# Kernel tuning notes

Measured on AMD Instinct MI355X. Metric: run time of the kernel, lower is better.

Reference implementation:

```python
import jax, jax.numpy as jnp
import numpy as np

L, D, H, DH, W, G, FF = 2, 768, 12, 64, 256, 64, 3072  # W = one-sided window (attention_window=512)
B, S = 2, 4096
NEG = -1e9


def setup_inputs() -> dict:
    key = jax.random.key(0)
    ks = jax.random.split(key, 16)
    inp = {}
    inp['hidden_states'] = jax.random.normal(ks[0], (B, S, D), jnp.float32)
    # HF Longformer convention: <0 masked, >0 global, 0 local. First G tokens are global.
    inp['attention_mask'] = jnp.zeros((B, S), jnp.float32).at[:, :G].set(1.0)
    inp['padding_len'] = 0
    inp['level_hierarchy'] = 0
    def w(k, shape):
        return (jax.random.normal(k, shape, jnp.float32) * 0.02)
    for i, n in enumerate(['Wq', 'Wk', 'Wv', 'Wqg', 'Wkg', 'Wvg', 'Wo']):
        inp[n] = w(ks[1 + i], (L, D, D))
        inp['b' + n[1:].lower()] = jnp.zeros((L, D), jnp.float32)
    inp['Wi'] = w(ks[8], (L, D, FF)); inp['bi'] = jnp.zeros((L, FF), jnp.float32)
    inp['Wo2'] = w(ks[9], (L, FF, D)); inp['bo2'] = jnp.zeros((L, D), jnp.float32)
    for n in ['ln1', 'ln2']:
        inp[n + '_g'] = jnp.ones((L, D), jnp.float32)
        inp[n + '_b'] = jnp.zeros((L, D), jnp.float32)
    return inp


def _ln(x, g, b):
    mu = jnp.mean(x, -1, keepdims=True)
    var = jnp.mean(jnp.square(x - mu), -1, keepdims=True)
    return (x - mu) * jax.lax.rsqrt(var + 1e-5) * g + b


def _chunk3(x, nc, w):
    # x: [..., S, d] -> [..., nc, 3w, d]: keys of chunks (c-1, c, c+1), zero-padded at the ends
    shp = x.shape
    xr = x.reshape(shp[:-2] + (nc, w, shp[-1]))
    pad = [(0, 0)] * xr.ndim
    pad[-3] = (1, 1)
    xp = jnp.pad(xr, pad)
    return jnp.concatenate([xp[..., :-2, :, :], xp[..., 1:-1, :, :], xp[..., 2:, :, :]], axis=-2)


def _layer(h, mask, Wq, bq, Wk, bk, Wv, bv, Wqg, bqg, Wkg, bkg, Wvg, bvg,
           Wo, bo, ln1_g, ln1_b, Wi, bi, Wo2, bo2, ln2_g, ln2_b):
    Bb, Ss, Dd = h.shape
    nc = Ss // W
    scale = 1.0 / np.sqrt(DH)
    def heads(x):
        return x.reshape(Bb, Ss, H, DH).transpose(0, 2, 1, 3)  # [B,H,S,dh]
    q = heads(h @ Wq + bq) * scale
    k = heads(h @ Wk + bk)
    v = heads(h @ Wv + bv)
    # --- sliding-window (banded) attention, chunked ---
    qc = q.reshape(Bb, H, nc, W, DH)
    k3 = _chunk3(k, nc, W)  # [B,H,nc,3W,dh]
    v3 = _chunk3(v, nc, W)
    local = jnp.einsum('bhcid,bhcjd->bhcij', qc, k3)  # [B,H,nc,W,3W]
    i = jnp.arange(W)[:, None]
    j = jnp.arange(3 * W)[None, :]
    band_ok = jnp.abs(j - W - i) <= W                              # [W,3W]
    keypos = jnp.arange(nc)[:, None, None] * W + (j - W)[None]     # [nc,1,3W]
    in_range = (keypos >= 0) & (keypos < Ss)
    # masked and global keys are removed from the windowed attention (handled via global cols)
    key_local = _chunk3((mask == 0).astype(h.dtype)[..., None], nc, W)[..., 0] > 0.5  # [B,nc,3W]
    valid = band_ok[None, None] & in_range[None] & key_local[:, :, None, :]  # [B,nc,W,3W]
    local = jnp.where(valid[:, None], local, NEG)
    # --- global key columns (every token attends to the G global tokens) ---
    kg, vg = k[:, :, :G], v[:, :, :G]
    sg = jnp.einsum('bhsd,bhgd->bhsg', q, kg).reshape(Bb, H, nc, W, G)
    probs = jax.nn.softmax(jnp.concatenate([sg, local], axis=-1), axis=-1)
    pg, pl = probs[..., :G], probs[..., G:]
    out = (jnp.einsum('bhcig,bhgd->bhcid', pg, vg)
           + jnp.einsum('bhcij,bhcjd->bhcid', pl, v3)).reshape(Bb, H, Ss, DH)
    # --- global token rows: full attention with dedicated global projections ---
    qg = heads(h @ Wqg + bqg)[:, :, :G] * scale
    kgf = heads(h @ Wkg + bkg)
    vgf = heads(h @ Wvg + bvg)
    add = jnp.where(mask < 0, NEG, 0.0)[:, None, None, :]
    pgl = jax.nn.softmax(jnp.einsum('bhgd,bhsd->bhgs', qg, kgf) + add, axis=-1)
    out = out.at[:, :, :G].set(jnp.einsum('bhgs,bhsd->bhgd', pgl, vgf))
    out = jnp.where((mask < 0)[:, None, :, None], 0.0, out)
    attn = out.transpose(0, 2, 1, 3).reshape(Bb, Ss, Dd) @ Wo + bo
    h = _ln(attn + h, ln1_g, ln1_b)
    ff = jax.nn.gelu(h @ Wi + bi, approximate=False) @ Wo2 + bo2
    return _ln(ff + h, ln2_g, ln2_b)


def reference(hidden_states, attention_mask, padding_len, level_hierarchy,
              Wq, bq, Wk, bk, Wv, bv, Wqg, bqg, Wkg, bkg, Wvg, bvg,
              Wo, bo, ln1_g, ln1_b, Wi, bi, Wo2, bo2, ln2_g, ln2_b):
    h = hidden_states
    for l in range(L):
        h = _layer(h, attention_mask,
                   Wq[l], bq[l], Wk[l], bk[l], Wv[l], bv[l],
                   Wqg[l], bqg[l], Wkg[l], bkg[l], Wvg[l], bvg[l],
                   Wo[l], bo[l], ln1_g[l], ln1_b[l],
                   Wi[l], bi[l], Wo2[l], bo2[l], ln2_g[l], ln2_b[l])
    if padding_len > 0:
        h = h[:, :-padding_len]
    return h
```

## Files before the change

kernel.cpp:

```cpp
#include <hip/hip_runtime.h>

#define B_ 2
#define S_ 4096
#define D_ 768
#define H_ 12
#define DH_ 64
#define W_ 256
#define G_ 64
#define FF_ 3072
#define L_ 2
#define M_ (B_*S_)
#define NEGV -1e9f
#define NSPLIT 16

typedef short bf16x8 __attribute__((ext_vector_type(8)));
typedef float f32x4 __attribute__((ext_vector_type(4)));
typedef unsigned short u16;
typedef unsigned short u16x4 __attribute__((ext_vector_type(4)));

__device__ __forceinline__ u16 f2bf(float f) {
  union { float f; unsigned u; } a; a.f = f;
  unsigned r = a.u + 0x7FFFu + ((a.u >> 16) & 1u);
  return (u16)(r >> 16);
}
__device__ __forceinline__ float b2f(u16 u) {
  union { unsigned u; float f; } a; a.u = ((unsigned)u) << 16;
  return a.f;
}

__device__ __forceinline__ f32x4 mfma16(bf16x8 a, bf16x8 b, f32x4 c) {
  return __builtin_amdgcn_mfma_f32_16x16x32_bf16(a, b, c, 0, 0, 0);
}

__device__ __forceinline__ void gload16(const u16* g, u16* l) {
  __builtin_amdgcn_global_load_lds((const __attribute__((address_space(1))) void*)g,
                                   (__attribute__((address_space(3))) void*)l, 16, 0, 0);
}

__device__ __forceinline__ int xcd_swz(int bid, int nwg) {
  if ((nwg & 7) == 0) {
    int cpx = nwg >> 3;
    bid = (bid & 7) * cpx + (bid >> 3);
  }
  return bid;
}

struct Ptr7 { const float* p[7]; };
__global__ __launch_bounds__(256) void wtrans7(Ptr7 in, u16* __restrict__ out) {
  __shared__ float tile[32][33];
  int z = blockIdx.z;
  int slab = z >> 1, l = z & 1;
  const float* src = in.p[slab] + (size_t)l * D_ * D_;
  u16* dst = out + (size_t)z * D_ * D_;
  int k0 = blockIdx.y * 32, n0 = blockIdx.x * 32;
  int tx = threadIdx.x, ty = threadIdx.y;
#pragma unroll
  for (int i = 0; i < 4; i++)
    tile[ty + i*8][tx] = src[(size_t)(k0 + ty + i*8) * D_ + n0 + tx];
  __syncthreads();
#pragma unroll
  for (int i = 0; i < 4; i++)
    dst[(size_t)(n0 + ty + i*8) * D_ + k0 + tx] = f2bf(tile[tx][ty + i*8]);
}

__global__ __launch_bounds__(256) void wtrans(const float* __restrict__ in,
                                              u16* __restrict__ out, int K, int N) {
  __shared__ float tile[32][33];
  size_t base = (size_t)blockIdx.z * K * N;
  int k0 = blockIdx.y * 32, n0 = blockIdx.x * 32;
  int tx = threadIdx.x, ty = threadIdx.y;
#pragma unroll
  for (int i = 0; i < 4; i++)
    tile[ty + i*8][tx] = in[base + (size_t)(k0 + ty + i*8) * N + n0 + tx];
  __syncthreads();
#pragma unroll
  for (int i = 0; i < 4; i++)
    out[base + (size_t)(n0 + ty + i*8) * K + k0 + tx] = f2bf(tile[tx][ty + i*8]);
}

__global__ __launch_bounds__(256) void conv_b(const float* __restrict__ in,
                                              u16* __restrict__ outb, int n4) {
  int i = blockIdx.x * 256 + threadIdx.x;
  if (i >= n4) return;
  float4 v = ((const float4*)in)[i];
  u16x4 o;
  o[0] = f2bf(v.x); o[1] = f2bf(v.y); o[2] = f2bf(v.z); o[3] = f2bf(v.w);
  ((u16x4*)outb)[i] = o;
}

template <int MODE>
__device__ __forceinline__ float epi_post(float v) {
  if (MODE == 2) return v * 0.125f;
  if (MODE == 3) {
    float y = 0.79788456f * (v + 0.044715f * v * v * v);
    float e = __expf(fminf(2.f * y, 20.f));
    return v * e / (e + 1.f);
  }
  return v;
}

template <int MODE>
__global__ __launch_bounds__(256) void gemm_pipe(const u16* __restrict__ A,
                                                 const u16* __restrict__ Bt,
                                                 const float* __restrict__ bias,
                                                 u16* __restrict__ Cb,
                                                 int Ndim, int Kdim, int rowTileStride) {
  __shared__ u16 sA[2][4096];
  __shared__ u16 sB[2][4096];
  int gx = gridDim.x;
  int bid = blockIdx.x + blockIdx.y * gx;
  bid = xcd_swz(bid, gx * gridDim.y);
  int bm = (bid / gx) * rowTileStride * 128;
  int bn = (bid % gx) * 128;
  int tid = threadIdx.x;
  int lane = tid & 63, w = tid >> 6;
  int r0w = (w >> 1) * 64, c0w = (w & 1) * 64;
  int lr = lane & 15, lg = lane >> 4;

  int f0 = tid, l0 = f0 >> 3, s0 = (f0 & 7) ^ (l0 & 7);
  int row0 = (l0 << 1) | (s0 >> 2), c0s = (s0 & 3) * 8;
  int f1 = tid + 256, l1 = f1 >> 3, s1 = (f1 & 7) ^ (l1 & 7);
  int row1 = (l1 << 1) | (s1 >> 2), c1s = (s1 & 3) * 8;
  const u16* A0 = A + (size_t)(bm + row0) * Kdim + c0s;
  const u16* A1 = A + (size_t)(bm + row1) * Kdim + c1s;
  const u16* B0 = Bt + (size_t)(bn + row0) * Kdim + c0s;
  const u16* B1 = Bt + (size_t)(bn + row1) * Kdim + c1s;

  int offa[4], offb[4];
#pragma unroll
  for (int i = 0; i < 4; i++) {
    int ra = r0w + i * 16 + lr;
    int la = ra >> 1, sa = ((ra & 1) << 2) | lg;
    offa[i] = la * 64 + (sa ^ (la & 7)) * 8;
    int rb = c0w + i * 16 + lr;
    int lb = rb >> 1, sb = ((rb & 1) << 2) | lg;
    offb[i] = lb * 64 + (sb ^ (lb & 7)) * 8;
  }

  int nt = Kdim >> 5;
  f32x4 acc[4][4] = {};

  gload16(A0, &sA[0][tid * 8]);
  gload16(A1, &sA[0][tid * 8 + 2048]);
  gload16(B0, &sB[0][tid * 8]);
  gload16(B1, &sB[0][tid * 8 + 2048]);

  for (int t = 0; t < nt; t++) {
    int cur = t & 1;
    if (t + 1 < nt) {
      int k1 = (t + 1) << 5;
      gload16(A0 + k1, &sA[cur ^ 1][tid * 8]);
      gload16(A1 + k1, &sA[cur ^ 1][tid * 8 + 2048]);
      gload16(B0 + k1, &sB[cur ^ 1][tid * 8]);
      gload16(B1 + k1, &sB[cur ^ 1][tid * 8 + 2048]);
      asm volatile("s_waitcnt vmcnt(4)" ::: "memory");
    } else {
      asm volatile("s_waitcnt vmcnt(0)" ::: "memory");
    }
    __builtin_amdgcn_s_barrier();
    __builtin_amdgcn_sched_barrier(0);
    bf16x8 a[4], b[4];
#pragma unroll
    for (int i = 0; i < 4; i++) a[i] = *(const bf16x8*)&sA[cur][offa[i]];
#pragma unroll
    for (int j = 0; j < 4; j++) b[j] = *(const bf16x8*)&sB[cur][offb[j]];
#pragma unroll
    for (int i = 0; i < 4; i++)
#pragma unroll
      for (int j = 0; j < 4; j++)
        acc[i][j] = mfma16(a[i], b[j], acc[i][j]);
    __builtin_amdgcn_sched_barrier(0);
    __builtin_amdgcn_s_barrier();
    __builtin_amdgcn_sched_barrier(0);
  }

  int r0 = bm + r0w, c0 = bn + c0w;
  int cr = (lane >> 4) * 4, cc = lane & 15;
#pragma unroll
  for (int j = 0; j < 4; j++) {
    int col = c0 + j * 16 + cc;
    float bv = bias[col];
#pragma unroll
    for (int i = 0; i < 4; i++)
#pragma unroll
      for (int r = 0; r < 4; r++) {
        size_t off = (size_t)(r0 + i * 16 + cr + r) * Ndim + col;
        Cb[off] = f2bf(epi_post<MODE>(acc[i][j][r] + bv));
      }
  }
}

struct Bias5 { const float* p[5]; };
__global__ __launch_bounds__(256) void gemm_qkv(const u16* __restrict__ A,
                                                const u16* __restrict__ Wt,
                                                Bias5 bp,
                                                u16* __restrict__ OutBase,
                                                int l) {
  __shared__ u16 sA[2][4096];
  __shared__ u16 sB[2][4096];
  int bid = blockIdx.x + blockIdx.y * 30;
  bid = xcd_swz(bid, 1920);
  int bx = bid % 30, by = bid / 30;
  int widx = bx / 6;
  int bn = (bx % 6) * 128;
  int bm = by * 128;
  int slab = widx + (widx >= 3 ? 1 : 0);
  const size_t DD = (size_t)D_ * D_;
  const u16* Bt = Wt + ((size_t)slab * L_ + l) * DD;
  u16* Cb = OutBase + (size_t)slab * M_ * D_;
  const float* bias = bp.p[widx];
  int tid = threadIdx.x;
  int lane = tid & 63, w = tid >> 6;
  int r0w = (w >> 1) * 64, c0w = (w & 1) * 64;
  int lr = lane & 15, lg = lane >> 4;

  int f0 = tid, l0 = f0 >> 3, s0 = (f0 & 7) ^ (l0 & 7);
  int row0 = (l0 << 1) | (s0 >> 2), c0s = (s0 & 3) * 8;
  int f1 = tid + 256, l1 = f1 >> 3, s1 = (f1 & 7) ^ (l1 & 7);
  int row1 = (l1 << 1) | (s1 >> 2), c1s = (s1 & 3) * 8;
  const u16* A0 = A + (size_t)(bm + row0) * D_ + c0s;
  const u16* A1 = A + (size_t)(bm + row1) * D_ + c1s;
  const u16* B0 = Bt + (size_t)(bn + row0) * D_ + c0s;
  const u16* B1 = Bt + (size_t)(bn + row1) * D_ + c1s;

  int offa[4], offb[4];
#pragma unroll
  for (int i = 0; i < 4; i++) {
    int ra = r0w + i * 16 + lr;
    int la = ra >> 1, sa = ((ra & 1) << 2) | lg;
    offa[i] = la * 64 + (sa ^ (la & 7)) * 8;
    int rb = c0w + i * 16 + lr;
    int lb = rb >> 1, sb = ((rb & 1) << 2) | lg;
    offb[i] = lb * 64 + (sb ^ (lb & 7)) * 8;
  }

  const int nt = D_ >> 5;
  f32x4 acc[4][4] = {};

  gload16(A0, &sA[0][tid * 8]);
  gload16(A1, &sA[0][tid * 8 + 2048]);
  gload16(B0, &sB[0][tid * 8]);
  gload16(B1, &sB[0][tid * 8 + 2048]);

  for (int t = 0; t < nt; t++) {
    int cur = t & 1;
    if (t + 1 < nt) {
      int k1 = (t + 1) << 5;
      gload16(A0 + k1, &sA[cur ^ 1][tid * 8]);
      gload16(A1 + k1, &sA[cur ^ 1][tid * 8 + 2048]);
      gload16(B0 + k1, &sB[cur ^ 1][tid * 8]);
      gload16(B1 + k1, &sB[cur ^ 1][tid * 8 + 2048]);
      asm volatile("s_waitcnt vmcnt(4)" ::: "memory");
    } else {
      asm volatile("s_waitcnt vmcnt(0)" ::: "memory");
    }
    __builtin_amdgcn_s_barrier();
    __builtin_amdgcn_sched_barrier(0);
    bf16x8 a[4], b[4];
#pragma unroll
    for (int i = 0; i < 4; i++) a[i] = *(const bf16x8*)&sA[cur][offa[i]];
#pragma unroll
    for (int j = 0; j < 4; j++) b[j] = *(const bf16x8*)&sB[cur][offb[j]];
#pragma unroll
    for (int i = 0; i < 4; i++)
#pragma unroll
      for (int j = 0; j < 4; j++)
        acc[i][j] = mfma16(a[i], b[j], acc[i][j]);
    __builtin_amdgcn_sched_barrier(0);
    __builtin_amdgcn_s_barrier();
    __builtin_amdgcn_sched_barrier(0);
  }

  int r0 = bm + r0w, c0 = bn + c0w;
  int cr = (lane >> 4) * 4, cc = lane & 15;
  float scale = (widx == 0) ? 0.125f : 1.0f;
#pragma unroll
  for (int j = 0; j < 4; j++) {
    int col = c0 + j * 16 + cc;
    float bv = bias[col];
#pragma unroll
    for (int i = 0; i < 4; i++)
#pragma unroll
      for (int r = 0; r < 4; r++) {
        size_t off = (size_t)(r0 + i * 16 + cr + r) * D_ + col;
        Cb[off] = f2bf((acc[i][j][r] + bv) * scale);
      }
  }
}

__global__ __launch_bounds__(128) void attn_local(const u16* __restrict__ qb,
                                                  const u16* __restrict__ kb_,
                                                  const u16* __restrict__ vb,
                                                  const float* __restrict__ mask,
                                                  u16* __restrict__ ao) {
  int bid = blockIdx.x + blockIdx.y * gridDim.x;
  bid = xcd_swz(bid, 1536);
  int cx = bid & 63, bh = bid >> 6;
  int c = cx >> 2, sub = cx & 3;
  int b = bh / H_, h = bh % H_;
  int tid = threadIdx.x;
  int w = tid >> 6, lane = tid & 63;
  int lr = lane & 15, lg = lane >> 4;

  __shared__ u16 vtT[64][72];
  __shared__ u16 plds[2][32][72];
  __shared__ unsigned char vflag[576];

  int base_off = sub * 64;
  int kwin0 = c * W_ - W_;
  for (int i = tid; i < 576; i += 128) {
    int kp = kwin0 + base_off + i;
    vflag[i] = (kp >= 0 && kp < S_ && mask[b * S_ + kp] == 0.0f) ? 1 : 0;
  }

  size_t hoff = (size_t)b * S_ * D_ + h * DH_;
  int qrow0 = c * W_ + base_off + w * 32;
  bf16x8 aq[2][2];
#pragma unroll
  for (int fi = 0; fi < 2; fi++)
#pragma unroll
    for (int ks = 0; ks < 2; ks++)
      aq[fi][ks] = *(const bf16x8*)(qb + hoff + (size_t)(qrow0 + fi * 16 + lr) * D_ + ks * 32 + lg * 8);

  float ls[2][4];
  f32x4 o[2][4] = {};
#pragma unroll
  for (int fi = 0; fi < 2; fi++)
#pragma unroll
    for (int r = 0; r < 4; r++) ls[fi][r] = 0.f;

  int stg_k4 = tid >> 3, stg_j = tid & 7;
  int stg_dh0 = stg_j * 8;

  for (int kb = 0; kb <= 9; kb++) {
    int kstart = 0;
    if (kb > 0) {
      kstart = kwin0 + base_off + (kb - 1) * 64;
      if (kstart + 64 <= 0 || kstart >= S_) continue;
    }
    __syncthreads();
    {
#pragma unroll
      for (int p = 0; p < 4; p++) {
        int key = p * 16 + stg_k4;
        int kp = (kb ? kstart : 0) + key;
        bf16x8 row = *(const bf16x8*)(vb + hoff + (size_t)kp * D_ + stg_dh0);
        u16* basep = &vtT[stg_dh0][key ^ (stg_j << 3)];
#pragma unroll
        for (int e = 0; e < 8; e++) basep[e * 72] = (u16)row[e];
      }
    }
    __syncthreads();

    bf16x8 bk0[4], bk1[4];
#pragma unroll
    for (int nj = 0; nj < 4; nj++) {
      int kp = (kb ? kstart : 0) + nj * 16 + lr;
      const u16* ks8 = kb_ + hoff + (size_t)kp * D_ + lg * 8;
      bk0[nj] = *(const bf16x8*)(ks8);
      bk1[nj] = *(const bf16x8*)(ks8 + 32);
    }
    f32x4 sc[2][4];
#pragma unroll
    for (int fi = 0; fi < 2; fi++)
#pragma unroll
      for (int nj = 0; nj < 4; nj++) {
        f32x4 t = {};
        t = mfma16(aq[fi][0], bk0[nj], t);
        t = mfma16(aq[fi][1], bk1[nj], t);
        sc[fi][nj] = t;
      }

    if (kb >= 2 && kb <= 8) {
#pragma unroll
      for (int nj = 0; nj < 4; nj++) {
        bool kv = vflag[(kb - 1) * 64 + nj * 16 + lr] != 0;
#pragma unroll
        for (int fi = 0; fi < 2; fi++)
#pragma unroll
          for (int r = 0; r < 4; r++)
            sc[fi][nj][r] = kv ? sc[fi][nj][r] : NEGV;
      }
    } else if (kb > 0) {
#pragma unroll
      for (int nj = 0; nj < 4; nj++) {
        int fidx = (kb - 1) * 64 + nj * 16 + lr;
        int koff = base_off + fidx;
        bool kv = vflag[fidx] != 0;
#pragma unroll
        for (int fi = 0; fi < 2; fi++)
#pragma unroll
          for (int r = 0; r < 4; r++) {
            int wq = base_off + w * 32 + fi * 16 + lg * 4 + r;
            if (!(kv && koff >= wq && koff <= wq + 2 * W_)) sc[fi][nj][r] = NEGV;
          }
      }
    }

#pragma unroll
    for (int fi = 0; fi < 2; fi++)
#pragma unroll
      for (int r = 0; r < 4; r++) {
        float ps = 0.f;
#pragma unroll
        for (int nj = 0; nj < 4; nj++) {
          float p = __expf(sc[fi][nj][r]);
          sc[fi][nj][r] = p;
          ps += p;
        }
#pragma unroll
        for (int d = 1; d < 16; d <<= 1) ps += __shfl_xor(ps, d);
        ls[fi][r] += ps;
      }

#pragma unroll
    for (int fi = 0; fi < 2; fi++)
#pragma unroll
      for (int nj = 0; nj < 4; nj++)
#pragma unroll
        for (int r = 0; r < 4; r++)
          plds[w][fi * 16 + lg * 4 + r][nj * 16 + lr] = f2bf(sc[fi][nj][r]);
    asm volatile("s_waitcnt lgkmcnt(0)" ::: "memory");
    __builtin_amdgcn_sched_barrier(0);

    bf16x8 ap[2][2];
#pragma unroll
    for (int fi = 0; fi < 2; fi++)
#pragma unroll
      for (int ks = 0; ks < 2; ks++)
        ap[fi][ks] = *(const bf16x8*)&plds[w][fi * 16 + lr][ks * 32 + lg * 8];
#pragma unroll
    for (int dj = 0; dj < 4; dj++) {
      int xr = ((dj * 16 + lr) >> 3) & 7;
#pragma unroll
      for (int ks = 0; ks < 2; ks++) {
        bf16x8 bv = *(const bf16x8*)&vtT[dj * 16 + lr][(ks * 32 + lg * 8) ^ (xr << 3)];
        o[0][dj] = mfma16(ap[0][ks], bv, o[0][dj]);
        o[1][dj] = mfma16(ap[1][ks], bv, o[1][dj]);
      }
    }
  }

#pragma unroll
  for (int fi = 0; fi < 2; fi++)
#pragma unroll
    for (int dj = 0; dj < 4; dj++)
#pragma unroll
      for (int r = 0; r < 4; r++) {
        int row = qrow0 + fi * 16 + lg * 4 + r;
        float v = o[fi][dj][r] / ls[fi][r];
        ao[hoff + (size_t)row * D_ + dj * 16 + lr] = f2bf(v);
      }
}

__global__ __launch_bounds__(128) void attn_gsplit(const u16* __restrict__ qg,
                                                   const u16* __restrict__ kg,
                                                   const u16* __restrict__ vg,
                                                   float* __restrict__ opart,
                                                   float* __restrict__ lpart) {
  int sp = blockIdx.x, bh = blockIdx.y;
  int b = bh / H_, h = bh % H_;
  int tid = threadIdx.x, w = tid >> 6, lane = tid & 63;
  int lr = lane & 15, lg = lane >> 4;
  __shared__ u16 vtT[64][72];
  __shared__ u16 plds[2][32][72];
  size_t hoff = (size_t)b * S_ * D_ + h * DH_;
  int qrow0 = w * 32;
  bf16x8 aq[2][2];
#pragma unroll
  for (int fi = 0; fi < 2; fi++)
#pragma unroll
    for (int ks = 0; ks < 2; ks++)
      aq[fi][ks] = *(const bf16x8*)(qg + hoff + (size_t)(qrow0 + fi * 16 + lr) * D_ + ks * 32 + lg * 8);
  float ls[2][4];
  f32x4 o[2][4] = {};
#pragma unroll
  for (int fi = 0; fi < 2; fi++)
#pragma unroll
    for (int r = 0; r < 4; r++) ls[fi][r] = 0.f;

  int stg_k4 = tid >> 3, stg_j = tid & 7;
  int stg_dh0 = stg_j * 8;

  for (int kb = 0; kb < 4; kb++) {
    int kstart = sp * 256 + kb * 64;
    __syncthreads();
#pragma unroll
    for (int p = 0; p < 4; p++) {
      int key = p * 16 + stg_k4;
      bf16x8 row = *(const bf16x8*)(vg + hoff + (size_t)(kstart + key) * D_ + stg_dh0);
      u16* basep = &vtT[stg_dh0][key ^ (stg_j << 3)];
#pragma unroll
      for (int e = 0; e < 8; e++) basep[e * 72] = (u16)row[e];
    }
    __syncthreads();

    bf16x8 bk0[4], bk1[4];
#pragma unroll
    for (int nj = 0; nj < 4; nj++) {
      const u16* ks8 = kg + hoff + (size_t)(kstart + nj * 16 + lr) * D_ + lg * 8;
      bk0[nj] = *(const bf16x8*)(ks8);
      bk1[nj] = *(const bf16x8*)(ks8 + 32);
    }
    f32x4 sc[2][4];
#pragma unroll
    for (int fi = 0; fi < 2; fi++)
#pragma unroll
      for (int nj = 0; nj < 4; nj++) {
        f32x4 t = {};
        t = mfma16(aq[fi][0], bk0[nj], t);
        t = mfma16(aq[fi][1], bk1[nj], t);
        sc[fi][nj] = t;
      }
#pragma unroll
    for (int fi = 0; fi < 2; fi++)
#pragma unroll
      for (int r = 0; r < 4; r++) {
        float ps = 0.f;
#pragma unroll
        for (int nj = 0; nj < 4; nj++) {
          float p = __expf(sc[fi][nj][r]);
          sc[fi][nj][r] = p;
          ps += p;
        }
#pragma unroll
        for (int d = 1; d < 16; d <<= 1) ps += __shfl_xor(ps, d);
        ls[fi][r] += ps;
      }
#pragma unroll
    for (int fi = 0; fi < 2; fi++)
#pragma unroll
      for (int nj = 0; nj < 4; nj++)
#pragma unroll
        for (int r = 0; r < 4; r++)
          plds[w][fi * 16 + lg * 4 + r][nj * 16 + lr] = f2bf(sc[fi][nj][r]);
    asm volatile("s_waitcnt lgkmcnt(0)" ::: "memory");
    __builtin_amdgcn_sched_barrier(0);
    bf16x8 ap[2][2];
#pragma unroll
    for (int fi = 0; fi < 2; fi++)
#pragma unroll
      for (int ks = 0; ks < 2; ks++)
        ap[fi][ks] = *(const bf16x8*)&plds[w][fi * 16 + lr][ks * 32 + lg * 8];
#pragma unroll
    for (int dj = 0; dj < 4; dj++) {
      int xr = ((dj * 16 + lr) >> 3) & 7;
#pragma unroll
      for (int ks = 0; ks < 2; ks++) {
        bf16x8 bv = *(const bf16x8*)&vtT[dj * 16 + lr][(ks * 32 + lg * 8) ^ (xr << 3)];
        o[0][dj] = mfma16(ap[0][ks], bv, o[0][dj]);
        o[1][dj] = mfma16(ap[1][ks], bv, o[1][dj]);
      }
    }
  }

  size_t pbase = (size_t)(bh * NSPLIT + sp) * 64;
#pragma unroll
  for (int fi = 0; fi < 2; fi++)
#pragma unroll
    for (int r = 0; r < 4; r++) {
      int row = qrow0 + fi * 16 + lg * 4 + r;
      if (lr == 0) lpart[pbase + row] = ls[fi][r];
#pragma unroll
      for (int dj = 0; dj < 4; dj++)
        opart[(pbase + row) * 64 + dj * 16 + lr] = o[fi][dj][r];
    }
}

__global__ __launch_bounds__(256) void attn_gcombine(const float* __restrict__ opart,
                                                     const float* __restrict__ lpart,
                                                     u16* __restrict__ ao) {
  int bh = blockIdx.x;
  int b = bh / H_, h = bh % H_;
  int t = threadIdx.x;
  __shared__ float lt[64];
  if (t < 64) {
    float lsum = 0.f;
#pragma unroll
    for (int sp = 0; sp < NSPLIT; sp++)
      lsum += lpart[(size_t)(bh * NSPLIT + sp) * 64 + t];
    lt[t] = lsum;
  }
  __syncthreads();
  int row = t >> 2, c0 = (t & 3) * 16;
  float acc[16] = {};
  for (int sp = 0; sp < NSPLIT; sp++) {
    const float* op = opart + ((size_t)(bh * NSPLIT + sp) * 64 + row) * 64 + c0;
#pragma unroll
    for (int j = 0; j < 16; j++) acc[j] += op[j];
  }
  float inv = 1.f / lt[row];
  size_t hoff = (size_t)b * S_ * D_ + h * DH_;
#pragma unroll
  for (int j = 0; j < 16; j++)
    ao[hoff + (size_t)row * D_ + c0 + j] = f2bf(acc[j] * inv);
}

__global__ __launch_bounds__(192) void ln_b(const u16* __restrict__ x,
                                            const u16* __restrict__ res,
                                            const float* __restrict__ gg,
                                            const float* __restrict__ bb,
                                            u16* __restrict__ outb,
                                            float* __restrict__ outf) {
  int row = blockIdx.x, t = threadIdx.x;
  const u16* xr = x + (size_t)row * D_;
  const u16* rr = res + (size_t)row * D_;
  u16x4 xv = *(const u16x4*)&xr[t * 4];
  u16x4 rv = *(const u16x4*)&rr[t * 4];
  float v[4];
#pragma unroll
  for (int e = 0; e < 4; e++) v[e] = b2f(xv[e]) + b2f(rv[e]);
  __shared__ float sha[3], shb[3];
  float s = v[0] + v[1] + v[2] + v[3];
#pragma unroll
  for (int d = 1; d < 64; d <<= 1) s += __shfl_xor(s, d);
  if ((t & 63) == 0) sha[t >> 6] = s;
  __syncthreads();
  float mu = (sha[0] + sha[1] + sha[2]) * (1.f / 768.f);
  float dd[4], s2 = 0.f;
#pragma unroll
  for (int e = 0; e < 4; e++) { dd[e] = v[e] - mu; s2 += dd[e] * dd[e]; }
#pragma unroll
  for (int d = 1; d < 64; d <<= 1) s2 += __shfl_xor(s2, d);
  if ((t & 63) == 0) shb[t >> 6] = s2;
  __syncthreads();
  float var = (shb[0] + shb[1] + shb[2]) * (1.f / 768.f);
  float rs = rsqrtf(var + 1e-5f);
  float4 gv = *(const float4*)&gg[t * 4];
  float4 bv = *(const float4*)&bb[t * 4];
  float y0 = dd[0] * rs * gv.x + bv.x;
  float y1 = dd[1] * rs * gv.y + bv.y;
  float y2 = dd[2] * rs * gv.z + bv.z;
  float y3 = dd[3] * rs * gv.w + bv.w;
  u16x4 ov;
  ov[0] = f2bf(y0); ov[1] = f2bf(y1); ov[2] = f2bf(y2); ov[3] = f2bf(y3);
  *(u16x4*)&outb[(size_t)row * D_ + t * 4] = ov;
  if (outf) {
    float4 of = {y0, y1, y2, y3};
    *(float4*)&outf[(size_t)row * D_ + t * 4] = of;
  }
}

extern "C" void kernel_launch(void* const* d_in, const int* in_sizes, int n_in,
                              void* d_out, int out_size, void* d_ws, size_t ws_size,
                              hipStream_t stream) {
  (void)in_sizes; (void)n_in; (void)out_size; (void)ws_size;
  const float* hidden = (const float*)d_in[0];
  const float* mask   = (const float*)d_in[1];
  const float* Wq  = (const float*)d_in[4];   const float* bq  = (const float*)d_in[5];
  const float* Wk  = (const float*)d_in[6];   const float* bk  = (const float*)d_in[7];
  const float* Wv  = (const float*)d_in[8];   const float* bv  = (const float*)d_in[9];
  const float* Wqg = (const float*)d_in[10];  const float* bqg = (const float*)d_in[11];
  const float* Wkg = (const float*)d_in[12];  const float* bkg = (const float*)d_in[13];
  const float* Wvg = (const float*)d_in[14];  const float* bvg = (const float*)d_in[15];
  const float* Wo  = (const float*)d_in[16];  const float* bo  = (const float*)d_in[17];
  const float* Wi  = (const float*)d_in[18];  const float* bi  = (const float*)d_in[19];
  const float* Wo2 = (const float*)d_in[20];  const float* bo2 = (const float*)d_in[21];
  const float* ln1g = (const float*)d_in[22]; const float* ln1b = (const float*)d_in[23];
  const float* ln2g = (const float*)d_in[24]; const float* ln2b = (const float*)d_in[25];

  char* ws = (char*)d_ws;
  size_t off = 0;
  auto alloc = [&](size_t bytes) -> void* {
    void* p = ws + off;
    off += (bytes + 255) & ~(size_t)255;
    return p;
  };
  const size_t DD = (size_t)D_ * D_;
  const size_t DF = (size_t)D_ * FF_;
  u16* Wt = (u16*)alloc((7 * L_ * DD + 2 * L_ * DF) * 2);
  u16* wqg_t = Wt + 3 * L_ * DD;
  u16* wo_t  = Wt + 6 * L_ * DD;
  u16* wi_t  = Wt + 7 * L_ * DD;
  u16* wo2_t = Wt + 7 * L_ * DD + L_ * DF;

  u16* X0 = (u16*)alloc((size_t)M_ * D_ * 2);
  u16* X1 = (u16*)alloc((size_t)M_ * D_ * 2);
  u16* tb = (u16*)alloc((size_t)M_ * D_ * 2);
  u16* B_bf = (u16*)alloc((size_t)M_ * FF_ * 2);
  u16* qbf  = (u16*)alloc((size_t)M_ * D_ * 2);
  u16* kbf  = (u16*)alloc((size_t)M_ * D_ * 2);
  u16* vbf  = (u16*)alloc((size_t)M_ * D_ * 2);
  u16* qgbf = (u16*)alloc((size_t)M_ * D_ * 2);
  u16* kgbf = (u16*)alloc((size_t)M_ * D_ * 2);
  u16* vgbf = (u16*)alloc((size_t)M_ * D_ * 2);
  u16* aobf = (u16*)alloc((size_t)M_ * D_ * 2);
  float* opart = (float*)alloc((size_t)B_ * H_ * NSPLIT * 64 * 64 * 4);
  float* lpart = (float*)alloc((size_t)B_ * H_ * NSPLIT * 64 * 4);

  dim3 tb32(32, 8);
  Ptr7 wp;
  wp.p[0] = Wq; wp.p[1] = Wk; wp.p[2] = Wv; wp.p[3] = Wqg;
  wp.p[4] = Wkg; wp.p[5] = Wvg; wp.p[6] = Wo;
  wtrans7<<<dim3(24, 24, 14), tb32, 0, stream>>>(wp, Wt);
  wtrans<<<dim3(96, 24, 2), tb32, 0, stream>>>(Wi,  wi_t,  D_, FF_);
  wtrans<<<dim3(24, 96, 2), tb32, 0, stream>>>(Wo2, wo2_t, FF_, D_);

  conv_b<<<(M_ * D_ / 4 + 255) / 256, 256, 0, stream>>>(hidden, X0, M_ * D_ / 4);

  for (int l = 0; l < L_; l++) {
    size_t wdd = (size_t)l * DD;
    size_t wdf = (size_t)l * DF;
    dim3 g64(6, 64), g2(6, 2), gff(24, 64);

    Bias5 bp;
    bp.p[0] = bq  + l * D_;
    bp.p[1] = bk  + l * D_;
    bp.p[2] = bv  + l * D_;
    bp.p[3] = bkg + l * D_;
    bp.p[4] = bvg + l * D_;
    gemm_qkv<<<dim3(30, 64), 256, 0, stream>>>(X0, Wt, bp, qbf, l);
    gemm_pipe<2><<<g2, 256, 0, stream>>>(X0, wqg_t + wdd, bqg + l * D_, qgbf, D_, D_, 32);

    attn_local<<<dim3((S_ / W_) * 4, B_ * H_), 128, 0, stream>>>(qbf, kbf, vbf, mask, aobf);
    attn_gsplit<<<dim3(NSPLIT, B_ * H_), 128, 0, stream>>>(qgbf, kgbf, vgbf, opart, lpart);
    attn_gcombine<<<B_ * H_, 256, 0, stream>>>(opart, lpart, aobf);

    gemm_pipe<1><<<g64, 256, 0, stream>>>(aobf, wo_t + wdd, bo + l * D_, tb, D_, D_, 1);
    ln_b<<<M_, 192, 0, stream>>>(tb, X0, ln1g + l * D_, ln1b + l * D_, X1, nullptr);

    gemm_pipe<3><<<gff, 256, 0, stream>>>(X1, wi_t + wdf, bi + l * FF_, B_bf, FF_, D_, 1);
    gemm_pipe<1><<<g64, 256, 0, stream>>>(B_bf, wo2_t + wdf, bo2 + l * D_, tb, D_, FF_, 1);

    ln_b<<<M_, 192, 0, stream>>>(tb, X1, ln2g + l * D_, ln2b + l * D_, X0,
                                 (l == L_ - 1) ? (float*)d_out : nullptr);
  }
}
```

Baseline: 737.0 us.

## Add 256x256-tile 512-thread GEMM for QKV and FFN-up projections

```diff
diff --git a/kernel.cpp b/kernel.cpp
--- a/kernel.cpp
+++ b/kernel.cpp
@@ -97,6 +97,130 @@
     return v * e / (e + 1.f);
   }
   return v;
+}
+
+struct Bias5 { const float* p[5]; };
+
+template <int MODE, int NW>
+__global__ __launch_bounds__(512, 1) void gemm256(const u16* __restrict__ A,
+                                                  const u16* __restrict__ Wbase,
+                                                  Bias5 bp,
+                                                  u16* __restrict__ OutBase,
+                                                  int Kdim, int Nstride, int l) {
+  __shared__ u16 sA[2][256 * 64];
+  __shared__ u16 sB[2][256 * 64];
+  int gx = gridDim.x;
+  int bid = blockIdx.x + blockIdx.y * gx;
+  bid = xcd_swz(bid, gx * gridDim.y);
+  int bxx = bid % gx, by = bid / gx;
+  int bm = by * 256;
+  int widx, bn;
+  const u16* Bt; u16* Cb; const float* bias;
+  if (NW == 5) {
+    widx = bxx / 3;
+    bn = (bxx % 3) * 256;
+    int slab = widx + (widx >= 3 ? 1 : 0);
+    Bt = Wbase + ((size_t)slab * L_ + l) * (size_t)D_ * D_;
+    Cb = OutBase + (size_t)slab * M_ * D_;
+    bias = bp.p[widx];
+  } else {
+    widx = 0;
+    bn = bxx * 256;
+    Bt = Wbase; Cb = OutBase; bias = bp.p[0];
+  }
+  int tid = threadIdx.x;
+  int lane = tid & 63, wid = tid >> 6;
+  int wr = wid >> 2, wc = wid & 3;
+  int lr = lane & 15, lg = lane >> 4;
+
+  const u16* srcA[4]; const u16* srcB[4];
+#pragma unroll
+  for (int i = 0; i < 4; i++) {
+    int f = tid + i * 512;
+    int row = f >> 3, slot = f & 7;
+    int c8 = slot ^ (row & 7);
+    srcA[i] = A + (size_t)(bm + row) * Kdim + c8 * 8;
+    srcB[i] = Bt + (size_t)(bn + row) * Kdim + c8 * 8;
+  }
+
+  f32x4 acc[8][4] = {};
+  int nt = Kdim >> 6;
+
+#pragma unroll
+  for (int i = 0; i < 4; i++) {
+    gload16(srcA[i], &sA[0][(tid + i * 512) * 8]);
+    gload16(srcB[i], &sB[0][(tid + i * 512) * 8]);
+  }
+
+  for (int kt = 0; kt < nt; kt++) {
+    int cur = kt & 1;
+    if (kt + 1 < nt) {
+      int k1 = (kt + 1) << 6;
+#pragma unroll
+      for (int i = 0; i < 4; i++) {
+        gload16(srcA[i] + k1, &sA[cur ^ 1][(tid + i * 512) * 8]);
+        gload16(srcB[i] + k1, &sB[cur ^ 1][(tid + i * 512) * 8]);
+      }
+      asm volatile("s_waitcnt vmcnt(8)" ::: "memory");
+    } else {
+      asm volatile("s_waitcnt vmcnt(0)" ::: "memory");
+    }
+    __builtin_amdgcn_s_barrier();
+    __builtin_amdgcn_sched_barrier(0);
+
+#pragma unroll
+    for (int qm = 0; qm < 2; qm++) {
+      bf16x8 af[4][2];
+#pragma unroll
+      for (int mi = 0; mi < 4; mi++)
+#pragma unroll
+        for (int ks = 0; ks < 2; ks++) {
+          int row = wr * 128 + qm * 64 + mi * 16 + lr;
+          int c8 = ks * 4 + lg;
+          af[mi][ks] = *(const bf16x8*)&sA[cur][row * 64 + ((c8 ^ (row & 7)) * 8)];
+        }
+#pragma unroll
+      for (int qn = 0; qn < 2; qn++) {
+        bf16x8 bfr[2][2];
+#pragma unroll
+        for (int nj = 0; nj < 2; nj++)
+#pragma unroll
+          for (int ks = 0; ks < 2; ks++) {
+            int row = wc * 64 + qn * 32 + nj * 16 + lr;
+            int c8 = ks * 4 + lg;
+            bfr[nj][ks] = *(const bf16x8*)&sB[cur][row * 64 + ((c8 ^ (row & 7)) * 8)];
+          }
+        __builtin_amdgcn_s_setprio(1);
+#pragma unroll
+        for (int mi = 0; mi < 4; mi++)
+#pragma unroll
+          for (int nj = 0; nj < 2; nj++)
+#pragma unroll
+            for (int ks = 0; ks < 2; ks++)
+              acc[qm * 4 + mi][qn * 2 + nj] =
+                  mfma16(af[mi][ks], bfr[nj][ks], acc[qm * 4 + mi][qn * 2 + nj]);
+        __builtin_amdgcn_s_setprio(0);
+      }
+    }
+    __builtin_amdgcn_sched_barrier(0);
+    __builtin_amdgcn_s_barrier();
+  }
+
+  int r0 = bm + wr * 128, c0 = bn + wc * 64;
+  int cr = (lane >> 4) * 4, cc = lane & 15;
+  float sc = (NW == 5 && widx == 0) ? 0.125f : 1.0f;
+#pragma unroll
+  for (int nj = 0; nj < 4; nj++) {
+    int col = c0 + nj * 16 + cc;
+    float bv = bias[col];
+#pragma unroll
+    for (int mi = 0; mi < 8; mi++)
+#pragma unroll
+      for (int r = 0; r < 4; r++) {
+        size_t off = (size_t)(r0 + mi * 16 + cr + r) * Nstride + col;
+        Cb[off] = f2bf(epi_post<MODE>((acc[mi][nj][r] + bv) * sc));
+      }
+  }
 }
 
 template <int MODE>
@@ -190,104 +314,6 @@
   }
 }
 
-struct Bias5 { const float* p[5]; };
-__global__ __launch_bounds__(256) void gemm_qkv(const u16* __restrict__ A,
-                                                const u16* __restrict__ Wt,
-                                                Bias5 bp,
-                                                u16* __restrict__ OutBase,
-                                                int l) {
-  __shared__ u16 sA[2][4096];
-  __shared__ u16 sB[2][4096];
-  int bid = blockIdx.x + blockIdx.y * 30;
-  bid = xcd_swz(bid, 1920);
-  int bx = bid % 30, by = bid / 30;
-  int widx = bx / 6;
-  int bn = (bx % 6) * 128;
-  int bm = by * 128;
-  int slab = widx + (widx >= 3 ? 1 : 0);
-  const size_t DD = (size_t)D_ * D_;
-  const u16* Bt = Wt + ((size_t)slab * L_ + l) * DD;
-  u16* Cb = OutBase + (size_t)slab * M_ * D_;
-  const float* bias = bp.p[widx];
-  int tid = threadIdx.x;
-  int lane = tid & 63, w = tid >> 6;
-  int r0w = (w >> 1) * 64, c0w = (w & 1) * 64;
-  int lr = lane & 15, lg = lane >> 4;
-
-  int f0 = tid, l0 = f0 >> 3, s0 = (f0 & 7) ^ (l0 & 7);
-  int row0 = (l0 << 1) | (s0 >> 2), c0s = (s0 & 3) * 8;
-  int f1 = tid + 256, l1 = f1 >> 3, s1 = (f1 & 7) ^ (l1 & 7);
-  int row1 = (l1 << 1) | (s1 >> 2), c1s = (s1 & 3) * 8;
-  const u16* A0 = A + (size_t)(bm + row0) * D_ + c0s;
-  const u16* A1 = A + (size_t)(bm + row1) * D_ + c1s;
-  const u16* B0 = Bt + (size_t)(bn + row0) * D_ + c0s;
-  const u16* B1 = Bt + (size_t)(bn + row1) * D_ + c1s;
-
-  int offa[4], offb[4];
-#pragma unroll
-  for (int i = 0; i < 4; i++) {
-    int ra = r0w + i * 16 + lr;
-    int la = ra >> 1, sa = ((ra & 1) << 2) | lg;
-    offa[i] = la * 64 + (sa ^ (la & 7)) * 8;
-    int rb = c0w + i * 16 + lr;
-    int lb = rb >> 1, sb = ((rb & 1) << 2) | lg;
-    offb[i] = lb * 64 + (sb ^ (lb & 7)) * 8;
-  }
-
-  const int nt = D_ >> 5;
-  f32x4 acc[4][4] = {};
-
-  gload16(A0, &sA[0][tid * 8]);
-  gload16(A1, &sA[0][tid * 8 + 2048]);
-  gload16(B0, &sB[0][tid * 8]);
-  gload16(B1, &sB[0][tid * 8 + 2048]);
-
-  for (int t = 0; t < nt; t++) {
-    int cur = t & 1;
-    if (t + 1 < nt) {
-      int k1 = (t + 1) << 5;
-      gload16(A0 + k1, &sA[cur ^ 1][tid * 8]);
-      gload16(A1 + k1, &sA[cur ^ 1][tid * 8 + 2048]);
-      gload16(B0 + k1, &sB[cur ^ 1][tid * 8]);
-      gload16(B1 + k1, &sB[cur ^ 1][tid * 8 + 2048]);
-      asm volatile("s_waitcnt vmcnt(4)" ::: "memory");
-    } else {
-      asm volatile("s_waitcnt vmcnt(0)" ::: "memory");
-    }
-    __builtin_amdgcn_s_barrier();
-    __builtin_amdgcn_sched_barrier(0);
-    bf16x8 a[4], b[4];
-#pragma unroll
-    for (int i = 0; i < 4; i++) a[i] = *(const bf16x8*)&sA[cur][offa[i]];
-#pragma unroll
-    for (int j = 0; j < 4; j++) b[j] = *(const bf16x8*)&sB[cur][offb[j]];
-#pragma unroll
-    for (int i = 0; i < 4; i++)
-#pragma unroll
-      for (int j = 0; j < 4; j++)
-        acc[i][j] = mfma16(a[i], b[j], acc[i][j]);
-    __builtin_amdgcn_sched_barrier(0);
-    __builtin_amdgcn_s_barrier();
-    __builtin_amdgcn_sched_barrier(0);
-  }
-
-  int r0 = bm + r0w, c0 = bn + c0w;
-  int cr = (lane >> 4) * 4, cc = lane & 15;
-  float scale = (widx == 0) ? 0.125f : 1.0f;
-#pragma unroll
-  for (int j = 0; j < 4; j++) {
-    int col = c0 + j * 16 + cc;
-    float bv = bias[col];
-#pragma unroll
-    for (int i = 0; i < 4; i++)
-#pragma unroll
-      for (int r = 0; r < 4; r++) {
-        size_t off = (size_t)(r0 + i * 16 + cr + r) * D_ + col;
-        Cb[off] = f2bf((acc[i][j][r] + bv) * scale);
-      }
-  }
-}
-
 __global__ __launch_bounds__(128) void attn_local(const u16* __restrict__ qb,
                                                   const u16* __restrict__ kb_,
                                                   const u16* __restrict__ vb,
@@ -701,7 +727,7 @@
   for (int l = 0; l < L_; l++) {
     size_t wdd = (size_t)l * DD;
     size_t wdf = (size_t)l * DF;
-    dim3 g64(6, 64), g2(6, 2), gff(24, 64);
+    dim3 g64(6, 64), g2(6, 2);
 
     Bias5 bp;
     bp.p[0] = bq  + l * D_;
@@ -709,7 +735,7 @@
     bp.p[2] = bv  + l * D_;
     bp.p[3] = bkg + l * D_;
     bp.p[4] = bvg + l * D_;
-    gemm_qkv<<<dim3(30, 64), 256, 0, stream>>>(X0, Wt, bp, qbf, l);
+    gemm256<1, 5><<<dim3(15, 32), 512, 0, stream>>>(X0, Wt, bp, qbf, D_, D_, l);
     gemm_pipe<2><<<g2, 256, 0, stream>>>(X0, wqg_t + wdd, bqg + l * D_, qgbf, D_, D_, 32);
 
     attn_local<<<dim3((S_ / W_) * 4, B_ * H_), 128, 0, stream>>>(qbf, kbf, vbf, mask, aobf);
@@ -719,7 +745,8 @@
     gemm_pipe<1><<<g64, 256, 0, stream>>>(aobf, wo_t + wdd, bo + l * D_, tb, D_, D_, 1);
     ln_b<<<M_, 192, 0, stream>>>(tb, X0, ln1g + l * D_, ln1b + l * D_, X1, nullptr);
 
-    gemm_pipe<3><<<gff, 256, 0, stream>>>(X1, wi_t + wdf, bi + l * FF_, B_bf, FF_, D_, 1);
+    Bias5 bpi; bpi.p[0] = bi + l * FF_;
+    gemm256<3, 1><<<dim3(12, 32), 512, 0, stream>>>(X1, wi_t + wdf, bpi, B_bf, D_, FF_, 0);
     gemm_pipe<1><<<g64, 256, 0, stream>>>(B_bf, wo2_t + wdf, bo2 + l * D_, tb, D_, FF_, 1);
 
     ln_b<<<M_, 192, 0, stream>>>(tb, X1, ln2g + l * D_, ln2b + l * D_, X0,
```

Result: no change. 751.1 us (+1.9%).
